# Kernel optimization log

Hardware: AMD Instinct MI355X
Metric: run time of the kernel (lower is better)

## Reference

```python
import jax, jax.numpy as jnp
import numpy as np

N = 100000
E = 1600000
D_IN = 128
D_OUT = 128


def setup_inputs() -> dict:
    key = jax.random.key(0)
    k1, k2, k3, k4, k5 = jax.random.split(key, 5)
    X = jax.random.normal(k1, (N, D_IN), dtype=jnp.float32)
    # degrees holds d^{-1/2} style per-node normalization factors (positive)
    degrees = jax.random.uniform(k2, (N,), dtype=jnp.float32, minval=0.05, maxval=1.0)
    # CSR row pointers: sorted, anchored at 0 and E
    rp = jnp.sort(jax.random.randint(k3, (N + 1,), 0, E, dtype=jnp.int64))
    row_pointers = rp.at[0].set(0).at[-1].set(E)
    column_index = jax.random.randint(k4, (E,), 0, N, dtype=jnp.int64)
    # dense GCN weight, uniform(-stdv, stdv) with stdv = 1/sqrt(output_dim)
    stdv = 1.0 / np.sqrt(D_OUT)
    weights = jax.random.uniform(k5, (D_IN, D_OUT), dtype=jnp.float32, minval=-stdv, maxval=stdv)
    return {"X": X, "weights": weights, "degrees": degrees,
            "row_pointers": row_pointers, "column_index": column_index}


def _spmm_csr(row_pointers, column_index, degrees, H):
    """out[i] = sum_{e in row i} degrees[i]*degrees[col[e]] * H[col[e]] (symmetric GCN norm)."""
    n = row_pointers.shape[0] - 1
    e = column_index.shape[0]
    # map each edge to its destination row via the CSR pointer array
    row_id = jnp.searchsorted(row_pointers, jnp.arange(e), side="right") - 1  # [E]
    coef = degrees[row_id] * degrees[column_index]                             # [E]
    gathered = H[column_index] * coef[:, None]                                 # [E, D]
    return jax.ops.segment_sum(gathered, row_id, num_segments=n)               # [N, D]


def reference(X, weights, degrees, row_pointers, column_index):
    X_prime = X @ weights                      # dense projection [N, D_OUT]
    return _spmm_csr(row_pointers, column_index, degrees, X_prime)
```

## Files before the change

### kernel.cpp

```cpp
#include <hip/hip_runtime.h>
#include <hip/hip_bf16.h>

#define D 128

typedef __attribute__((ext_vector_type(8))) short bf16x8;
typedef __attribute__((ext_vector_type(4))) float f32x4;

static __device__ __forceinline__ ushort f2bf(float f) {
    __hip_bfloat16 h = __float2bfloat16(f);
    return *(ushort*)&h;
}
static __device__ __forceinline__ float bfl(uint u) { return __uint_as_float(u << 16); }
static __device__ __forceinline__ float bfh(uint u) { return __uint_as_float(u & 0xffff0000u); }

__global__ __launch_bounds__(256) void swizzle_w(const float* __restrict__ W,
                                                 ushort* __restrict__ Wz)
{
    const int t = blockIdx.x * 256 + threadIdx.x;
    const int lane = t & 63;
    const int combo = t >> 6;
    const int ks = combo >> 3, nb = combo & 7;
    const int krow = ks * 32 + ((lane >> 4) << 3);
    const int col  = nb * 16 + (lane & 15);
    ushort u[8];
    #pragma unroll
    for (int j = 0; j < 8; ++j) u[j] = f2bf(W[(krow + j) * D + col]);
    uint4 p;
    p.x = (uint)u[0] | ((uint)u[1] << 16);
    p.y = (uint)u[2] | ((uint)u[3] << 16);
    p.z = (uint)u[4] | ((uint)u[5] << 16);
    p.w = (uint)u[6] | ((uint)u[7] << 16);
    *(uint4*)(Wz + (size_t)t * 8) = p;
}

__global__ __launch_bounds__(256) void gemm_mfma(const float* __restrict__ X,
                                                 const ushort* __restrict__ Wz,
                                                 const float* __restrict__ deg,
                                                 ushort* __restrict__ Xp, int n)
{
    __shared__ ushort wsh[32 * 64 * 8];
    const int tid = threadIdx.x;
    {
        const uint4* src = (const uint4*)Wz;
        uint4* dst = (uint4*)wsh;
        #pragma unroll
        for (int i = 0; i < 8; ++i) dst[tid + i * 256] = src[tid + i * 256];
    }
    __syncthreads();

    const int lane = tid & 63;
    const int wave = tid >> 6;
    const int m = lane & 15, quad = lane >> 4;
    const int r0 = blockIdx.x * 128 + wave * 32;

    bf16x8 xfrag[2][4];
    #pragma unroll
    for (int t = 0; t < 2; ++t) {
        long long arow = r0 + t * 16 + m;
        if (arow >= n) arow = n - 1;
        const float* xa = X + arow * D + quad * 8;
        #pragma unroll
        for (int ks = 0; ks < 4; ++ks) {
            float4 lo = *(const float4*)(xa + ks * 32);
            float4 hi = *(const float4*)(xa + ks * 32 + 4);
            bf16x8 a;
            a[0] = (short)f2bf(lo.x); a[1] = (short)f2bf(lo.y);
            a[2] = (short)f2bf(lo.z); a[3] = (short)f2bf(lo.w);
            a[4] = (short)f2bf(hi.x); a[5] = (short)f2bf(hi.y);
            a[6] = (short)f2bf(hi.z); a[7] = (short)f2bf(hi.w);
            xfrag[t][ks] = a;
        }
    }

    f32x4 acc[2][8];
    #pragma unroll
    for (int t = 0; t < 2; ++t)
        #pragma unroll
        for (int nb = 0; nb < 8; ++nb) acc[t][nb] = (f32x4){0.f, 0.f, 0.f, 0.f};

    #pragma unroll
    for (int nb = 0; nb < 8; ++nb) {
        #pragma unroll
        for (int ks = 0; ks < 4; ++ks) {
            bf16x8 w = *(const bf16x8*)(wsh + ((size_t)((ks * 8 + nb) * 64 + lane)) * 8);
            acc[0][nb] = __builtin_amdgcn_mfma_f32_16x16x32_bf16(w, xfrag[0][ks], acc[0][nb], 0, 0, 0);
            acc[1][nb] = __builtin_amdgcn_mfma_f32_16x16x32_bf16(w, xfrag[1][ks], acc[1][nb], 0, 0, 0);
        }
    }

    #pragma unroll
    for (int t = 0; t < 2; ++t) {
        const int row = r0 + t * 16 + m;
        if (row < n) {
            const float dr = deg[row];
            ushort* dstrow = Xp + (size_t)row * D + quad * 4;
            #pragma unroll
            for (int nb = 0; nb < 8; ++nb) {
                uint2 p;
                p.x = (uint)f2bf(dr * acc[t][nb][0]) | ((uint)f2bf(dr * acc[t][nb][1]) << 16);
                p.y = (uint)f2bf(dr * acc[t][nb][2]) | ((uint)f2bf(dr * acc[t][nb][3]) << 16);
                *(uint2*)(dstrow + nb * 16) = p;
            }
        }
    }
}

__global__ __launch_bounds__(256) void spmm_csr(const ushort* __restrict__ Xp,
                                                const float* __restrict__ deg,
                                                const int* __restrict__ rp,
                                                const int* __restrict__ ci,
                                                float* __restrict__ out, int n)
{
    int row = __builtin_amdgcn_readfirstlane(blockIdx.x * 4 + (threadIdx.x >> 6));
    if (row >= n) row = n - 1;
    const int lane = threadIdx.x & 63;
    const int beg = rp[row];
    const int end = rp[row + 1];
    const uint* __restrict__ Xq = (const uint*)Xp;

    float a0 = 0.f, a1 = 0.f;
    float b0 = 0.f, b1 = 0.f;

    int e = beg;
    for (; e + 8 <= end; e += 8) {
        const int c0 = ci[e + 0], c1 = ci[e + 1], c2 = ci[e + 2], c3 = ci[e + 3];
        const int c4 = ci[e + 4], c5 = ci[e + 5], c6 = ci[e + 6], c7 = ci[e + 7];
        const uint v0 = Xq[(size_t)c0 * 64 + lane];
        const uint v1 = Xq[(size_t)c1 * 64 + lane];
        const uint v2 = Xq[(size_t)c2 * 64 + lane];
        const uint v3 = Xq[(size_t)c3 * 64 + lane];
        const uint v4 = Xq[(size_t)c4 * 64 + lane];
        const uint v5 = Xq[(size_t)c5 * 64 + lane];
        const uint v6 = Xq[(size_t)c6 * 64 + lane];
        const uint v7 = Xq[(size_t)c7 * 64 + lane];
        a0 += bfl(v0); a1 += bfh(v0);
        b0 += bfl(v1); b1 += bfh(v1);
        a0 += bfl(v2); a1 += bfh(v2);
        b0 += bfl(v3); b1 += bfh(v3);
        a0 += bfl(v4); a1 += bfh(v4);
        b0 += bfl(v5); b1 += bfh(v5);
        a0 += bfl(v6); a1 += bfh(v6);
        b0 += bfl(v7); b1 += bfh(v7);
    }

    if (e < end) {
        int cc[8];
        #pragma unroll
        for (int j = 0; j < 8; ++j) {
            const int ee = e + j;
            cc[j] = ci[ee < end ? ee : end - 1];
        }
        uint vv[8];
        #pragma unroll
        for (int j = 0; j < 8; ++j) vv[j] = Xq[(size_t)cc[j] * 64 + lane];
        #pragma unroll
        for (int j = 0; j < 8; ++j) {
            if (e + j < end) {
                a0 += bfl(vv[j]); a1 += bfh(vv[j]);
            }
        }
    }

    const float dr = deg[row];
    float2 o;
    o.x = dr * (a0 + b0);
    o.y = dr * (a1 + b1);
    *(float2*)(out + (size_t)row * D + lane * 2) = o;
}

extern "C" void kernel_launch(void* const* d_in, const int* in_sizes, int n_in,
                              void* d_out, int out_size, void* d_ws, size_t ws_size,
                              hipStream_t stream)
{
    const float* X   = (const float*)d_in[0];
    const float* W   = (const float*)d_in[1];
    const float* deg = (const float*)d_in[2];
    const int*   rp  = (const int*)d_in[3];
    const int*   ci  = (const int*)d_in[4];
    float* out = (float*)d_out;
    const int n = in_sizes[2];

    ushort* Xp = (ushort*)d_ws;
    ushort* Wz = Xp + (size_t)n * D;

    swizzle_w<<<8, 256, 0, stream>>>(W, Wz);
    gemm_mfma<<<(n + 127) / 128, 256, 0, stream>>>(X, Wz, deg, Xp, n);
    spmm_csr<<<(n + 3) / 4, 256, 0, stream>>>(Xp, deg, rp, ci, out, n);
}
```

Baseline: 176.3 us.

## Fuse weight swizzle, GEMM and SpMM into one persistent kernel with grid barrier

Replaces the three launches (weight swizzle, MFMA GEMM, CSR SpMM) with a single persistent kernel of 512 blocks. Each block swizzles W into shared memory, grid-strides over GEMM tiles, then meets the other blocks at an atomic grid-wide barrier before grid-striding over SpMM rows. This removes launch gaps and the separate Wz buffer. In exchange, every block redoes the weight conversion from global memory, the SpMM runs with fewer resident waves to hide gather latency, and correctness relies on all 512 blocks being co-resident.

```diff
diff --git a/kernel.cpp b/kernel.cpp
--- a/kernel.cpp
+++ b/kernel.cpp
@@ -2,6 +2,7 @@
 #include <hip/hip_bf16.h>
 
 #define D 128
+#define GRID_BLOCKS 512
 
 typedef __attribute__((ext_vector_type(8))) short bf16x8;
 typedef __attribute__((ext_vector_type(4))) float f32x4;
@@ -13,159 +14,161 @@
 static __device__ __forceinline__ float bfl(uint u) { return __uint_as_float(u << 16); }
 static __device__ __forceinline__ float bfh(uint u) { return __uint_as_float(u & 0xffff0000u); }
 
-__global__ __launch_bounds__(256) void swizzle_w(const float* __restrict__ W,
-                                                 ushort* __restrict__ Wz)
-{
-    const int t = blockIdx.x * 256 + threadIdx.x;
-    const int lane = t & 63;
-    const int combo = t >> 6;
-    const int ks = combo >> 3, nb = combo & 7;
-    const int krow = ks * 32 + ((lane >> 4) << 3);
-    const int col  = nb * 16 + (lane & 15);
-    ushort u[8];
-    #pragma unroll
-    for (int j = 0; j < 8; ++j) u[j] = f2bf(W[(krow + j) * D + col]);
-    uint4 p;
-    p.x = (uint)u[0] | ((uint)u[1] << 16);
-    p.y = (uint)u[2] | ((uint)u[3] << 16);
-    p.z = (uint)u[4] | ((uint)u[5] << 16);
-    p.w = (uint)u[6] | ((uint)u[7] << 16);
-    *(uint4*)(Wz + (size_t)t * 8) = p;
-}
-
-__global__ __launch_bounds__(256) void gemm_mfma(const float* __restrict__ X,
-                                                 const ushort* __restrict__ Wz,
-                                                 const float* __restrict__ deg,
-                                                 ushort* __restrict__ Xp, int n)
+__global__ __launch_bounds__(256, 2) void gcn_fused(const float* __restrict__ X,
+                                                    const float* __restrict__ W,
+                                                    const float* __restrict__ deg,
+                                                    const int* __restrict__ rp,
+                                                    const int* __restrict__ ci,
+                                                    ushort* __restrict__ Xp,
+                                                    uint* __restrict__ bar,
+                                                    float* __restrict__ out, int n)
 {
     __shared__ ushort wsh[32 * 64 * 8];
-    const int tid = threadIdx.x;
-    {
-        const uint4* src = (const uint4*)Wz;
-        uint4* dst = (uint4*)wsh;
+    const int tid  = threadIdx.x;
+    const int lane = tid & 63;
+    const int wave = tid >> 6;
+
+    #pragma unroll
+    for (int i = 0; i < 8; ++i) {
+        const int s     = tid + i * 256;
+        const int combo = s >> 6;
+        const int ks = combo >> 3, nb = combo & 7;
+        const int krow = ks * 32 + ((lane >> 4) << 3);
+        const int col  = nb * 16 + (lane & 15);
+        ushort u[8];
         #pragma unroll
-        for (int i = 0; i < 8; ++i) dst[tid + i * 256] = src[tid + i * 256];
+        for (int j = 0; j < 8; ++j) u[j] = f2bf(W[(krow + j) * D + col]);
+        uint4 p;
+        p.x = (uint)u[0] | ((uint)u[1] << 16);
+        p.y = (uint)u[2] | ((uint)u[3] << 16);
+        p.z = (uint)u[4] | ((uint)u[5] << 16);
+        p.w = (uint)u[6] | ((uint)u[7] << 16);
+        ((uint4*)wsh)[s] = p;
     }
     __syncthreads();
 
-    const int lane = tid & 63;
-    const int wave = tid >> 6;
     const int m = lane & 15, quad = lane >> 4;
-    const int r0 = blockIdx.x * 128 + wave * 32;
+    const int ntiles = (n + 127) >> 7;
 
-    bf16x8 xfrag[2][4];
-    #pragma unroll
-    for (int t = 0; t < 2; ++t) {
-        long long arow = r0 + t * 16 + m;
-        if (arow >= n) arow = n - 1;
-        const float* xa = X + arow * D + quad * 8;
+    for (int tile = blockIdx.x; tile < ntiles; tile += GRID_BLOCKS) {
+        const int r0 = tile * 128 + wave * 32;
+
+        bf16x8 xfrag[2][4];
         #pragma unroll
-        for (int ks = 0; ks < 4; ++ks) {
-            float4 lo = *(const float4*)(xa + ks * 32);
-            float4 hi = *(const float4*)(xa + ks * 32 + 4);
-            bf16x8 a;
-            a[0] = (short)f2bf(lo.x); a[1] = (short)f2bf(lo.y);
-            a[2] = (short)f2bf(lo.z); a[3] = (short)f2bf(lo.w);
-            a[4] = (short)f2bf(hi.x); a[5] = (short)f2bf(hi.y);
-            a[6] = (short)f2bf(hi.z); a[7] = (short)f2bf(hi.w);
-            xfrag[t][ks] = a;
-        }
-    }
-
-    f32x4 acc[2][8];
-    #pragma unroll
-    for (int t = 0; t < 2; ++t)
-        #pragma unroll
-        for (int nb = 0; nb < 8; ++nb) acc[t][nb] = (f32x4){0.f, 0.f, 0.f, 0.f};
-
-    #pragma unroll
-    for (int nb = 0; nb < 8; ++nb) {
-        #pragma unroll
-        for (int ks = 0; ks < 4; ++ks) {
-            bf16x8 w = *(const bf16x8*)(wsh + ((size_t)((ks * 8 + nb) * 64 + lane)) * 8);
-            acc[0][nb] = __builtin_amdgcn_mfma_f32_16x16x32_bf16(w, xfrag[0][ks], acc[0][nb], 0, 0, 0);
-            acc[1][nb] = __builtin_amdgcn_mfma_f32_16x16x32_bf16(w, xfrag[1][ks], acc[1][nb], 0, 0, 0);
-        }
-    }
-
-    #pragma unroll
-    for (int t = 0; t < 2; ++t) {
-        const int row = r0 + t * 16 + m;
-        if (row < n) {
-            const float dr = deg[row];
-            ushort* dstrow = Xp + (size_t)row * D + quad * 4;
+        for (int t = 0; t < 2; ++t) {
+            long long arow = r0 + t * 16 + m;
+            if (arow >= n) arow = n - 1;
+            const float* xa = X + arow * D + quad * 8;
             #pragma unroll
-            for (int nb = 0; nb < 8; ++nb) {
-                uint2 p;
-                p.x = (uint)f2bf(dr * acc[t][nb][0]) | ((uint)f2bf(dr * acc[t][nb][1]) << 16);
-                p.y = (uint)f2bf(dr * acc[t][nb][2]) | ((uint)f2bf(dr * acc[t][nb][3]) << 16);
-                *(uint2*)(dstrow + nb * 16) = p;
+            for (int ks = 0; ks < 4; ++ks) {
+                float4 lo = *(const float4*)(xa + ks * 32);
+                float4 hi = *(const float4*)(xa + ks * 32 + 4);
+                bf16x8 a;
+                a[0] = (short)f2bf(lo.x); a[1] = (short)f2bf(lo.y);
+                a[2] = (short)f2bf(lo.z); a[3] = (short)f2bf(lo.w);
+                a[4] = (short)f2bf(hi.x); a[5] = (short)f2bf(hi.y);
+                a[6] = (short)f2bf(hi.z); a[7] = (short)f2bf(hi.w);
+                xfrag[t][ks] = a;
             }
         }
-    }
-}
 
-__global__ __launch_bounds__(256) void spmm_csr(const ushort* __restrict__ Xp,
-                                                const float* __restrict__ deg,
-                                                const int* __restrict__ rp,
-                                                const int* __restrict__ ci,
-                                                float* __restrict__ out, int n)
-{
-    int row = __builtin_amdgcn_readfirstlane(blockIdx.x * 4 + (threadIdx.x >> 6));
-    if (row >= n) row = n - 1;
-    const int lane = threadIdx.x & 63;
-    const int beg = rp[row];
-    const int end = rp[row + 1];
-    const uint* __restrict__ Xq = (const uint*)Xp;
+        f32x4 acc[2][8];
+        #pragma unroll
+        for (int t = 0; t < 2; ++t)
+            #pragma unroll
+            for (int nb = 0; nb < 8; ++nb) acc[t][nb] = (f32x4){0.f, 0.f, 0.f, 0.f};
 
-    float a0 = 0.f, a1 = 0.f;
-    float b0 = 0.f, b1 = 0.f;
+        #pragma unroll
+        for (int nb = 0; nb < 8; ++nb) {
+            #pragma unroll
+            for (int ks = 0; ks < 4; ++ks) {
+                bf16x8 w = *(const bf16x8*)(wsh + ((size_t)((ks * 8 + nb) * 64 + lane)) * 8);
+                acc[0][nb] = __builtin_amdgcn_mfma_f32_16x16x32_bf16(w, xfrag[0][ks], acc[0][nb], 0, 0, 0);
+                acc[1][nb] = __builtin_amdgcn_mfma_f32_16x16x32_bf16(w, xfrag[1][ks], acc[1][nb], 0, 0, 0);
+            }
+        }
 
-    int e = beg;
-    for (; e + 8 <= end; e += 8) {
-        const int c0 = ci[e + 0], c1 = ci[e + 1], c2 = ci[e + 2], c3 = ci[e + 3];
-        const int c4 = ci[e + 4], c5 = ci[e + 5], c6 = ci[e + 6], c7 = ci[e + 7];
-        const uint v0 = Xq[(size_t)c0 * 64 + lane];
-        const uint v1 = Xq[(size_t)c1 * 64 + lane];
-        const uint v2 = Xq[(size_t)c2 * 64 + lane];
-        const uint v3 = Xq[(size_t)c3 * 64 + lane];
-        const uint v4 = Xq[(size_t)c4 * 64 + lane];
-        const uint v5 = Xq[(size_t)c5 * 64 + lane];
-        const uint v6 = Xq[(size_t)c6 * 64 + lane];
-        const uint v7 = Xq[(size_t)c7 * 64 + lane];
-        a0 += bfl(v0); a1 += bfh(v0);
-        b0 += bfl(v1); b1 += bfh(v1);
-        a0 += bfl(v2); a1 += bfh(v2);
-        b0 += bfl(v3); b1 += bfh(v3);
-        a0 += bfl(v4); a1 += bfh(v4);
-        b0 += bfl(v5); b1 += bfh(v5);
-        a0 += bfl(v6); a1 += bfh(v6);
-        b0 += bfl(v7); b1 += bfh(v7);
-    }
-
-    if (e < end) {
-        int cc[8];
         #pragma unroll
-        for (int j = 0; j < 8; ++j) {
-            const int ee = e + j;
-            cc[j] = ci[ee < end ? ee : end - 1];
-        }
-        uint vv[8];
-        #pragma unroll
-        for (int j = 0; j < 8; ++j) vv[j] = Xq[(size_t)cc[j] * 64 + lane];
-        #pragma unroll
-        for (int j = 0; j < 8; ++j) {
-            if (e + j < end) {
-                a0 += bfl(vv[j]); a1 += bfh(vv[j]);
+        for (int t = 0; t < 2; ++t) {
+            const int row = r0 + t * 16 + m;
+            if (row < n) {
+                const float dr = deg[row];
+                ushort* dstrow = Xp + (size_t)row * D + quad * 4;
+                #pragma unroll
+                for (int nb = 0; nb < 8; ++nb) {
+                    uint2 p;
+                    p.x = (uint)f2bf(dr * acc[t][nb][0]) | ((uint)f2bf(dr * acc[t][nb][1]) << 16);
+                    p.y = (uint)f2bf(dr * acc[t][nb][2]) | ((uint)f2bf(dr * acc[t][nb][3]) << 16);
+                    *(uint2*)(dstrow + nb * 16) = p;
+                }
             }
         }
     }
 
-    const float dr = deg[row];
-    float2 o;
-    o.x = dr * (a0 + b0);
-    o.y = dr * (a1 + b1);
-    *(float2*)(out + (size_t)row * D + lane * 2) = o;
+    __syncthreads();
+    if (tid == 0) {
+        __threadfence();
+        __hip_atomic_fetch_add(bar, 1u, __ATOMIC_ACQ_REL, __HIP_MEMORY_SCOPE_AGENT);
+        while (__hip_atomic_load(bar, __ATOMIC_ACQUIRE, __HIP_MEMORY_SCOPE_AGENT) < (uint)GRID_BLOCKS)
+            __builtin_amdgcn_s_sleep(2);
+    }
+    __syncthreads();
+    (void)__hip_atomic_load(bar, __ATOMIC_ACQUIRE, __HIP_MEMORY_SCOPE_AGENT);
+
+    const uint* __restrict__ Xq = (const uint*)Xp;
+    const int ng = (n + 3) >> 2;
+
+    for (int g = blockIdx.x; g < ng; g += GRID_BLOCKS) {
+        const int row = __builtin_amdgcn_readfirstlane(g * 4 + wave);
+        if (row >= n) continue;
+        const int beg = rp[row], end = rp[row + 1];
+
+        float a0 = 0.f, a1 = 0.f, b0 = 0.f, b1 = 0.f;
+
+        int e = beg;
+        for (; e + 8 <= end; e += 8) {
+            const int c0 = ci[e + 0], c1 = ci[e + 1], c2 = ci[e + 2], c3 = ci[e + 3];
+            const int c4 = ci[e + 4], c5 = ci[e + 5], c6 = ci[e + 6], c7 = ci[e + 7];
+            const uint v0 = Xq[(size_t)c0 * 64 + lane];
+            const uint v1 = Xq[(size_t)c1 * 64 + lane];
+            const uint v2 = Xq[(size_t)c2 * 64 + lane];
+            const uint v3 = Xq[(size_t)c3 * 64 + lane];
+            const uint v4 = Xq[(size_t)c4 * 64 + lane];
+            const uint v5 = Xq[(size_t)c5 * 64 + lane];
+            const uint v6 = Xq[(size_t)c6 * 64 + lane];
+            const uint v7 = Xq[(size_t)c7 * 64 + lane];
+            a0 += bfl(v0); a1 += bfh(v0);
+            b0 += bfl(v1); b1 += bfh(v1);
+            a0 += bfl(v2); a1 += bfh(v2);
+            b0 += bfl(v3); b1 += bfh(v3);
+            a0 += bfl(v4); a1 += bfh(v4);
+            b0 += bfl(v5); b1 += bfh(v5);
+            a0 += bfl(v6); a1 += bfh(v6);
+            b0 += bfl(v7); b1 += bfh(v7);
+        }
+
+        if (e < end) {
+            int cc[8];
+            #pragma unroll
+            for (int j = 0; j < 8; ++j) {
+                const int ee = e + j;
+                cc[j] = ci[ee < end ? ee : end - 1];
+            }
+            uint vv[8];
+            #pragma unroll
+            for (int j = 0; j < 8; ++j) vv[j] = Xq[(size_t)cc[j] * 64 + lane];
+            #pragma unroll
+            for (int j = 0; j < 8; ++j) {
+                if (e + j < end) { a0 += bfl(vv[j]); a1 += bfh(vv[j]); }
+            }
+        }
+
+        const float dr = deg[row];
+        float2 o;
+        o.x = dr * (a0 + b0);
+        o.y = dr * (a1 + b1);
+        *(float2*)(out + (size_t)row * D + lane * 2) = o;
+    }
 }
 
 extern "C" void kernel_launch(void* const* d_in, const int* in_sizes, int n_in,
@@ -181,9 +184,8 @@
     const int n = in_sizes[2];
 
     ushort* Xp = (ushort*)d_ws;
-    ushort* Wz = Xp + (size_t)n * D;
+    uint*  bar = (uint*)(Xp + (size_t)n * D);
 
-    swizzle_w<<<8, 256, 0, stream>>>(W, Wz);
-    gemm_mfma<<<(n + 127) / 128, 256, 0, stream>>>(X, Wz, deg, Xp, n);
-    spmm_csr<<<(n + 3) / 4, 256, 0, stream>>>(Xp, deg, rp, ci, out, n);
+    hipMemsetAsync(bar, 0, sizeof(uint), stream);
+    gcn_fused<<<GRID_BLOCKS, 256, 0, stream>>>(X, W, deg, rp, ci, Xp, bar, out, n);
 }
```

Measured after the change: 356.0 us. 102% more time.

## Stage GEMM output through LDS for coalesced nontemporal stores, overlap weight load

Applied to the files above, without the earlier changes.

The GEMM kernel now loads the swizzled weights into registers before the X fragments are fetched and writes them to shared memory afterwards, so both global loads are in flight together. The scaled bf16 results are written into a padded 128x136 LDS tile and then stored as full contiguous 16-byte rows with nontemporal hints, replacing scattered 8-byte stores. The aim is more coalesced global writes and less exposed load latency, at the cost of extra LDS traffic, two more barriers and higher register pressure. The nontemporal hint also risks Xp being evicted from cache before the SpMM kernel gathers it.

```diff
diff --git a/kernel.cpp b/kernel.cpp
--- a/kernel.cpp
+++ b/kernel.cpp
@@ -5,6 +5,7 @@
 
 typedef __attribute__((ext_vector_type(8))) short bf16x8;
 typedef __attribute__((ext_vector_type(4))) float f32x4;
+typedef __attribute__((ext_vector_type(4))) uint  u32x4;
 
 static __device__ __forceinline__ ushort f2bf(float f) {
     __hip_bfloat16 h = __float2bfloat16(f);
@@ -38,18 +39,18 @@
                                                  const float* __restrict__ deg,
                                                  ushort* __restrict__ Xp, int n)
 {
-    __shared__ ushort wsh[32 * 64 * 8];
-    const int tid = threadIdx.x;
+    __shared__ ushort wsh[128 * 136];
+    const int tid  = threadIdx.x;
+    const int lane = tid & 63;
+    const int wave = tid >> 6;
+
+    uint4 wreg[8];
     {
         const uint4* src = (const uint4*)Wz;
-        uint4* dst = (uint4*)wsh;
-        #pragma unroll
-        for (int i = 0; i < 8; ++i) dst[tid + i * 256] = src[tid + i * 256];
-    }
-    __syncthreads();
-
-    const int lane = tid & 63;
-    const int wave = tid >> 6;
+        #pragma unroll
+        for (int i = 0; i < 8; ++i) wreg[i] = src[tid + i * 256];
+    }
+
     const int m = lane & 15, quad = lane >> 4;
     const int r0 = blockIdx.x * 128 + wave * 32;
 
@@ -72,6 +73,13 @@
         }
     }
 
+    {
+        uint4* dst = (uint4*)wsh;
+        #pragma unroll
+        for (int i = 0; i < 8; ++i) dst[tid + i * 256] = wreg[i];
+    }
+    __syncthreads();
+
     f32x4 acc[2][8];
     #pragma unroll
     for (int t = 0; t < 2; ++t)
@@ -88,19 +96,30 @@
         }
     }
 
+    __syncthreads();
     #pragma unroll
     for (int t = 0; t < 2; ++t) {
-        const int row = r0 + t * 16 + m;
-        if (row < n) {
-            const float dr = deg[row];
-            ushort* dstrow = Xp + (size_t)row * D + quad * 4;
+        const int lr   = wave * 32 + t * 16 + m;
+        const int grow = r0 + t * 16 + m;
+        const float dr = (grow < n) ? deg[grow] : 0.f;
+        #pragma unroll
+        for (int nb = 0; nb < 8; ++nb) {
+            uint2 p;
+            p.x = (uint)f2bf(dr * acc[t][nb][0]) | ((uint)f2bf(dr * acc[t][nb][1]) << 16);
+            p.y = (uint)f2bf(dr * acc[t][nb][2]) | ((uint)f2bf(dr * acc[t][nb][3]) << 16);
+            *(uint2*)(wsh + lr * 136 + nb * 16 + quad * 4) = p;
+        }
+    }
+    __syncthreads();
+    {
+        const int row  = tid >> 1, half = tid & 1;
+        const int grow = blockIdx.x * 128 + row;
+        if (grow < n) {
+            u32x4* dst = (u32x4*)(Xp + (size_t)grow * D + half * 64);
+            const ushort* src = wsh + row * 136 + half * 64;
             #pragma unroll
-            for (int nb = 0; nb < 8; ++nb) {
-                uint2 p;
-                p.x = (uint)f2bf(dr * acc[t][nb][0]) | ((uint)f2bf(dr * acc[t][nb][1]) << 16);
-                p.y = (uint)f2bf(dr * acc[t][nb][2]) | ((uint)f2bf(dr * acc[t][nb][3]) << 16);
-                *(uint2*)(dstrow + nb * 16) = p;
-            }
+            for (int i = 0; i < 8; ++i)
+                __builtin_nontemporal_store(*(const u32x4*)(src + i * 8), dst + i);
         }
     }
 }
@@ -155,9 +174,7 @@
         for (int j = 0; j < 8; ++j) vv[j] = Xq[(size_t)cc[j] * 64 + lane];
         #pragma unroll
         for (int j = 0; j < 8; ++j) {
-            if (e + j < end) {
-                a0 += bfl(vv[j]); a1 += bfh(vv[j]);
-            }
+            if (e + j < end) { a0 += bfl(vv[j]); a1 += bfh(vv[j]); }
         }
     }
 
```

Result: slower. 207.9 us (+17.9%).
